# Kernel tuning notes

Hardware: AMD Instinct MI355X
Metric: run time of the kernel (lower is better)

Reference implementation:

```python
import jax, jax.numpy as jnp
import numpy as np

B, T, C, H, N = 2, 1024, 2048, 32, 64
LAYER_ID, N_LAYERS = 12, 24
EPS = 1e-5 * 8 ** 2  # GroupNorm eps = 1e-5 * head_size_divisor**2


def setup_inputs() -> dict:
    key = jax.random.key(0)
    ks = jax.random.split(key, 16)
    nrm = lambda i, shape, s: jax.random.normal(ks[i], shape, jnp.float32) * s
    r01 = LAYER_ID / (N_LAYERS - 1)
    r1a0 = 1.0 - LAYER_ID / N_LAYERS
    ddd = (jnp.arange(C, dtype=jnp.float32) / C)[None, None, :]
    nn_ = jnp.arange(C, dtype=jnp.float32) / (C - 1)
    decay_speed = -7.0 + 5.0 * nn_ ** (0.85 + r01 ** 0.5)
    lin_s = 1.0 / float(np.sqrt(C))
    inp = dict(
        x=nrm(0, (B, T, C), 1.0),
        v_first=nrm(1, (B, T, C), 1.0),
        shift_state=jnp.zeros((B, C), jnp.float32),
        wkv_state=jnp.zeros((B, H, N, N), jnp.float32),
        x_r=1.0 - ddd ** (0.2 * r1a0),
        x_w=1.0 - ddd ** (0.9 * r1a0),
        x_k=1.0 - (ddd ** (0.9 * r1a0) + 0.4 * r01),
        x_v=1.0 - (ddd ** (0.4 * r1a0) + 0.6 * r01),
        x_a=1.0 - ddd ** (0.9 * r1a0),
        x_g=1.0 - ddd ** (0.2 * r1a0),
        w0=decay_speed[None, None, :] + 0.5,
        w1=nrm(2, (C, 64), 0.05), w2=nrm(3, (64, C), 0.1),
        a0=jnp.zeros((1, 1, C), jnp.float32),
        a1=nrm(4, (C, 64), 0.05), a2=nrm(5, (64, C), 0.1),
        v0=jnp.ones((1, 1, C), jnp.float32),
        v1=nrm(6, (C, 32), 0.05), v2=nrm(7, (32, C), 0.1),
        g1=nrm(8, (C, 128), 0.05), g2=nrm(9, (128, C), 0.1),
        k_k=jnp.full((1, 1, C), 0.85, jnp.float32),
        k_a=jnp.ones((1, 1, C), jnp.float32),
        r_k=nrm(10, (H, N), 0.02),
        W_r=nrm(11, (C, C), lin_s), W_k=nrm(12, (C, C), lin_s),
        W_v=nrm(13, (C, C), lin_s), W_o=nrm(14, (C, C), lin_s),
        ln_w=jnp.ones((C,), jnp.float32), ln_b=jnp.zeros((C,), jnp.float32),
    )
    return inp


def _forward(x, v_first, shift_state, wkv_state, x_r, x_w, x_k, x_v, x_a, x_g,
             w0, w1, w2, a0, a1, a2, v0, v1, v2, g1, g2, k_k, k_a, r_k,
             W_r, W_k, W_v, W_o, ln_w, ln_b):
    # token shift
    xx = jnp.concatenate([shift_state[:, None, :], x[:, :-1]], axis=1) - x
    xr, xw, xk, xv, xa, xg = (x + xx * m for m in (x_r, x_w, x_k, x_v, x_a, x_g))
    r = xr @ W_r
    k = xk @ W_k
    v = xv @ W_v
    # log-decay (strictly negative)
    w_log = -jax.nn.softplus(-(w0 + jnp.tanh(xw @ w1) @ w2)) - 0.5
    # residual value mixing towards layer-0 v (layer_id > 0 branch)
    v = v + (v_first - v) * jax.nn.sigmoid(v0 + xv @ v1 @ v2)
    a = jax.nn.sigmoid(a0 + xa @ a1 @ a2)
    g = jax.nn.sigmoid(xg @ g1) @ g2
    # per-head L2-normalized removal key
    kk = (k * k_k).reshape(B, T, H, N)
    kk = kk / jnp.maximum(jnp.linalg.norm(kk, axis=-1, keepdims=True), 1e-12)
    k2 = k * (1.0 + (a - 1.0) * k_a)
    # time-major [T,B,H,N] for the scan
    tm = lambda t: t.reshape(B, T, H, N).transpose(1, 0, 2, 3)
    rs, ks_, vs = tm(r), tm(k2), tm(v)
    ws = jnp.exp(tm(w_log))               # per-channel decay in (0,1)
    a_in = -kk.transpose(1, 0, 2, 3)      # removal direction
    b_in = (kk * a.reshape(B, T, H, N)).transpose(1, 0, 2, 3)
    def step(S, t):  # S: [B,H,Nv,Nk]
        r_, k_, v_, w_, a_, b_ = t
        sa = jnp.einsum('bhvk,bhk->bhv', S, a_)
        S = S * w_[:, :, None, :] \
            + jnp.einsum('bhv,bhk->bhvk', sa, b_) \
            + jnp.einsum('bhv,bhk->bhvk', v_, k_)
        return S, jnp.einsum('bhvk,bhk->bhv', S, r_)
    S_final, o = jax.lax.scan(step, wkv_state, (rs, ks_, vs, ws, a_in, b_in))
    o = o.transpose(1, 0, 2, 3)           # [B,T,H,N]
    # GroupNorm with H groups over C channels (per-head normalization)
    mu = o.mean(-1, keepdims=True)
    var = ((o - mu) ** 2).mean(-1, keepdims=True)
    on = ((o - mu) / jnp.sqrt(var + EPS)).reshape(B, T, C) * ln_w + ln_b
    # rkv bonus term
    rr, kr, vr = r.reshape(B, T, H, N), k2.reshape(B, T, H, N), v.reshape(B, T, H, N)
    bonus = ((rr * kr * r_k).sum(-1, keepdims=True) * vr).reshape(B, T, C)
    out = ((on + bonus) * g) @ W_o
    return out


def reference(x, v_first, shift_state, wkv_state, x_r, x_w, x_k, x_v, x_a, x_g,
              w0, w1, w2, a0, a1, a2, v0, v1, v2, g1, g2, k_k, k_a, r_k,
              W_r, W_k, W_v, W_o, ln_w, ln_b):
    return _forward(x, v_first, shift_state, wkv_state, x_r, x_w, x_k, x_v, x_a, x_g,
                    w0, w1, w2, a0, a1, a2, v0, v1, v2, g1, g2, k_k, k_a, r_k,
                    W_r, W_k, W_v, W_o, ln_w, ln_b)
```

## Files before the change

### kernel.cpp

```cpp
#include <hip/hip_runtime.h>
#include <cstdint>
#include <cstddef>


#define DI __device__ __forceinline__
static constexpr int T_ = 1024, C_ = 2048, H_ = 32;

typedef __attribute__((ext_vector_type(8))) __bf16 bf16x8;
typedef __attribute__((ext_vector_type(4))) float f32x4;
typedef __attribute__((ext_vector_type(8))) unsigned short us8v;
typedef __attribute__((ext_vector_type(4))) unsigned short us4v;
typedef __attribute__((ext_vector_type(2))) unsigned short us2v;

DI float sig_(float z) { return 1.0f / (1.0f + expf(-z)); }

DI unsigned short f2bf(float f) {
  union { float f; uint32_t u; } v; v.f = f;
  uint32_t u = v.u;
  return (unsigned short)((u + 0x7FFFu + ((u >> 16) & 1u)) >> 16);
}
DI float bf2f(unsigned short h) {
  union { uint32_t u; float f; } v; v.u = ((uint32_t)h) << 16;
  return v.f;
}

DI float dpp_xor1_add(float x) {
  int r = __builtin_amdgcn_update_dpp(0, __float_as_int(x), 0xB1, 0xF, 0xF, true);
  return x + __int_as_float(r);
}
DI float dpp_xor2_add(float x) {
  int r = __builtin_amdgcn_update_dpp(0, __float_as_int(x), 0x4E, 0xF, 0xF, true);
  return x + __int_as_float(r);
}
DI float dpp_hm_add(float x) {
  int r = __builtin_amdgcn_update_dpp(0, __float_as_int(x), 0x141, 0xF, 0xF, true);
  return x + __int_as_float(r);
}
DI float dpp_mir_add(float x) {
  int r = __builtin_amdgcn_update_dpp(0, __float_as_int(x), 0x140, 0xF, 0xF, true);
  return x + __int_as_float(r);
}

DI void gload16(const float* g, float* l) {
  __builtin_amdgcn_global_load_lds(
      (const __attribute__((address_space(1))) uint32_t*)g,
      (__attribute__((address_space(3))) uint32_t*)l, 16, 0, 0);
}
DI void gload16u(const unsigned short* g, unsigned short* l) {
  __builtin_amdgcn_global_load_lds(
      (const __attribute__((address_space(1))) uint32_t*)g,
      (__attribute__((address_space(3))) uint32_t*)l, 16, 0, 0);
}
DI void gload4(const float* g, float* l) {
  __builtin_amdgcn_global_load_lds(
      (const __attribute__((address_space(1))) uint32_t*)g,
      (__attribute__((address_space(3))) uint32_t*)l, 4, 0, 0);
}

struct Job {
  const float* A; const float* W; float* C; const float* bias;
  const float* mixv; const float* x; const float* shift;
  int N, K, ntn, aact, epi, tile_end;
};
struct Jobs { Job j[7]; };

__global__ __launch_bounds__(256) void gemm_oracle(Jobs P) {
  __shared__ float As[64][33];
  __shared__ float Ws[32][65];
  int bx = blockIdx.x, ji = 0;
  while (bx >= P.j[ji].tile_end) ++ji;
  Job J = P.j[ji];
  int tix = bx - (ji ? P.j[ji - 1].tile_end : 0);
  int mt = tix / J.ntn, nt = tix % J.ntn;
  int m0 = mt * 64, n0 = nt * 64;
  int tid = threadIdx.x, tx = tid & 15, ty = tid >> 4;
  float acc[4][4] = {};
  for (int k0 = 0; k0 < J.K; k0 += 32) {
    #pragma unroll
    for (int p = 0; p < 8; ++p) {
      int idx = p * 256 + tid;
      int r = idx >> 5, kc = idx & 31;
      int m = m0 + r, k = k0 + kc;
      float a;
      if (J.mixv) {
        float xv = J.x[(size_t)m * C_ + k];
        int t = m & (T_ - 1);
        float xp = (t == 0) ? J.shift[(size_t)(m >> 10) * C_ + k]
                            : J.x[(size_t)(m - 1) * C_ + k];
        a = xv + (xp - xv) * J.mixv[k];
      } else {
        a = J.A[(size_t)m * J.K + k];
        if (J.aact == 1) a = tanhf(a);
        else if (J.aact == 2) a = sig_(a);
      }
      As[r][kc] = a;
    }
    #pragma unroll
    for (int p = 0; p < 8; ++p) {
      int idx = p * 256 + tid;
      int kr = idx >> 6, nc = idx & 63;
      int n = n0 + nc;
      Ws[kr][nc] = (n < J.N) ? J.W[(size_t)(k0 + kr) * J.N + n] : 0.0f;
    }
    __syncthreads();
    #pragma unroll 4
    for (int kc = 0; kc < 32; ++kc) {
      float av[4], bv[4];
      #pragma unroll
      for (int i = 0; i < 4; ++i) av[i] = As[ty * 4 + i][kc];
      #pragma unroll
      for (int jn = 0; jn < 4; ++jn) bv[jn] = Ws[kc][tx * 4 + jn];
      #pragma unroll
      for (int i = 0; i < 4; ++i)
        #pragma unroll
        for (int jn = 0; jn < 4; ++jn) acc[i][jn] += av[i] * bv[jn];
    }
    __syncthreads();
  }
  #pragma unroll
  for (int i = 0; i < 4; ++i) {
    int rw = m0 + ty * 4 + i;
    #pragma unroll
    for (int jn = 0; jn < 4; ++jn) {
      int col = n0 + tx * 4 + jn;
      if (col < J.N) {
        float v = acc[i][jn];
        if (J.epi == 1) v = sig_(J.bias[col] + v);
        else if (J.epi == 2) v = 0.60653065971263342f * sig_(J.bias[col] + v);
        if (J.epi == 3) ((unsigned short*)J.C)[(size_t)rw * J.N + col] = f2bf(v);
        else            J.C[(size_t)rw * J.N + col] = v;
      }
    }
  }
}

struct TJob { const float* src; unsigned short* dh; unsigned short* dl; int N, ntn, tile_end; };
struct TJobs { TJob j[8]; };

__global__ __launch_bounds__(256) void wtrans(TJobs P) {
  __shared__ float t[64][65];
  int bx = blockIdx.x, ji = 0;
  while (bx >= P.j[ji].tile_end) ++ji;
  TJob J = P.j[ji];
  int tix = bx - (ji ? P.j[ji - 1].tile_end : 0);
  int kt = tix / J.ntn, nt = tix % J.ntn;
  int k0 = kt * 64, n0 = nt * 64;
  int tid = threadIdx.x;
  #pragma unroll
  for (int p = 0; p < 16; ++p) {
    int flat = p * 256 + tid;
    int r = flat >> 6, c = flat & 63;
    int n = n0 + c;
    t[r][c] = (n < J.N) ? J.src[(size_t)(k0 + r) * J.N + n] : 0.0f;
  }
  __syncthreads();
  #pragma unroll
  for (int p = 0; p < 8; ++p) {
    int flat = p * 256 + tid;
    int rr = flat >> 5, cc = (flat & 31) * 2;
    if (n0 + rr < J.N) {
      float w0v = t[cc][rr], w1v = t[cc + 1][rr];
      unsigned short h0 = f2bf(w0v), h1 = f2bf(w1v);
      us2v oh, ol;
      oh.x = h0; oh.y = h1;
      ol.x = f2bf(w0v - bf2f(h0));
      ol.y = f2bf(w1v - bf2f(h1));
      size_t off = (size_t)(n0 + rr) * 2048 + k0 + cc;
      *(us2v*)(J.dh + off) = oh;
      *(us2v*)(J.dl + off) = ol;
    }
  }
}

struct GJob {
  const float* A; const unsigned short* Wh; const unsigned short* Wl; float* C;
  const float* mixv; const float* shift;
  int N, K, ntn, kbeg, kend, atomicC, tile_end;
};
struct GJobs { GJob j[8]; };

__global__ __launch_bounds__(256, 2) void gemm_w256(GJobs P) {
  __shared__ unsigned short Ash[128][40];
  __shared__ unsigned short Asl[128][40];
  __shared__ unsigned short Bsh[256][32];
  __shared__ unsigned short Bsl[256][32];
  int bx = blockIdx.x, ji = 0;
  while (bx >= P.j[ji].tile_end) ++ji;
  GJob J = P.j[ji];
  int tix = bx - (ji ? P.j[ji - 1].tile_end : 0);
  int mt = tix / J.ntn, nt = tix % J.ntn;
  int m0 = mt * 128, n0 = nt * 256;
  int tid = threadIdx.x;
  int lane = tid & 63, wid = tid >> 6;
  int wr = wid >> 1, wc = wid & 1;
  int l15 = lane & 15, lg = lane >> 4;
  f32x4 acc[4][8] = {};

  int sr = tid >> 3, skq = tid & 7;
  float ax[4][4], aq[4][4], amv[4];

  auto loadA = [&](int k0) {
    int kk = k0 + skq * 4;
    if (J.mixv) *(float4*)amv = *(const float4*)(J.mixv + kk);
    #pragma unroll
    for (int p = 0; p < 4; ++p) {
      int m = m0 + p * 32 + sr;
      const float* xp0 = J.A + (size_t)m * J.K + kk;
      *(float4*)ax[p] = *(const float4*)xp0;
      if (J.mixv) {
        const float* pp = ((m & (T_ - 1)) == 0)
            ? (J.shift + (size_t)(m >> 10) * C_ + kk)
            : (xp0 - C_);
        *(float4*)aq[p] = *(const float4*)pp;
      }
    }
  };
  auto writeA = [&]() {
    #pragma unroll
    for (int p = 0; p < 4; ++p) {
      us4v oh, ol;
      #pragma unroll
      for (int q = 0; q < 4; ++q) {
        float va = J.mixv ? (ax[p][q] + (aq[p][q] - ax[p][q]) * amv[q]) : ax[p][q];
        unsigned short hq = f2bf(va);
        oh[q] = hq;
        ol[q] = f2bf(va - bf2f(hq));
      }
      int r = p * 32 + sr;
      *(us4v*)&Ash[r][skq * 4] = oh;
      *(us4v*)&Asl[r][skq * 4] = ol;
    }
  };
  auto stageB = [&](int k0) {
    #pragma unroll
    for (int j = 0; j < 4; ++j) {
      int r0 = wid * 64 + j * 16;
      int rdst = r0 + (lane >> 2);
      int nrow = n0 + rdst;
      if (nrow >= J.N) nrow = J.N - 1;
      int ssrc = (lane & 3) ^ ((rdst >> 1) & 3);
      size_t gofs = (size_t)nrow * J.K + k0 + ssrc * 8;
      gload16u(J.Wh + gofs, &Bsh[r0][0]);
      gload16u(J.Wl + gofs, &Bsl[r0][0]);
    }
  };

  loadA(J.kbeg);
  stageB(J.kbeg);
  writeA();
  asm volatile("s_waitcnt vmcnt(0)" ::: "memory");
  __syncthreads();

  for (int k0 = J.kbeg; k0 < J.kend; k0 += 32) {
    bool more = (k0 + 32 < J.kend);
    if (more) loadA(k0 + 32);
    bf16x8 afh[4], afl[4];
    #pragma unroll
    for (int i = 0; i < 4; ++i) {
      int rr = wr * 64 + i * 16 + l15;
      afh[i] = __builtin_bit_cast(bf16x8, *(const us8v*)&Ash[rr][lg * 8]);
      afl[i] = __builtin_bit_cast(bf16x8, *(const us8v*)&Asl[rr][lg * 8]);
    }
    #pragma unroll
    for (int jn = 0; jn < 8; ++jn) {
      int rb = wc * 128 + jn * 16 + l15;
      int sl = (lg ^ ((rb >> 1) & 3)) * 8;
      bf16x8 bh = __builtin_bit_cast(bf16x8, *(const us8v*)&Bsh[rb][sl]);
      bf16x8 bl = __builtin_bit_cast(bf16x8, *(const us8v*)&Bsl[rb][sl]);
      #pragma unroll
      for (int i = 0; i < 4; ++i) {
        acc[i][jn] = __builtin_amdgcn_mfma_f32_16x16x32_bf16(afh[i], bh, acc[i][jn], 0, 0, 0);
        acc[i][jn] = __builtin_amdgcn_mfma_f32_16x16x32_bf16(afl[i], bh, acc[i][jn], 0, 0, 0);
        acc[i][jn] = __builtin_amdgcn_mfma_f32_16x16x32_bf16(afh[i], bl, acc[i][jn], 0, 0, 0);
      }
    }
    __syncthreads();
    if (more) { stageB(k0 + 32); writeA(); }
    asm volatile("s_waitcnt vmcnt(0)" ::: "memory");
    __syncthreads();
  }

  int orow0 = m0 + wr * 64 + 4 * lg;
  int ocol0 = n0 + wc * 128 + l15;
  #pragma unroll
  for (int i = 0; i < 4; ++i) {
    #pragma unroll
    for (int jn = 0; jn < 8; ++jn) {
      int col = ocol0 + jn * 16;
      if (col < J.N) {
        #pragma unroll
        for (int rr = 0; rr < 4; ++rr) {
          size_t idx = (size_t)(orow0 + i * 16 + rr) * J.N + col;
          float v = acc[i][jn][rr];
          if (J.atomicC) atomicAdd(&J.C[idx], v);
          else           J.C[idx] = v;
        }
      }
    }
  }
}

__global__ __launch_bounds__(64) void prescan(
    float* __restrict__ kio, float* __restrict__ vio,
    float* __restrict__ amat_ain, float* __restrict__ vmix_bin,
    const float* __restrict__ vfirst,
    const float* __restrict__ k_k, const float* __restrict__ k_a) {
  __shared__ float red[64];
  int bid = blockIdx.x, tid = threadIdx.x;
  int h = bid & (H_ - 1);
  size_t base = (size_t)bid * 64 + tid;
  int cc = h * 64 + tid;
  float kv = kio[base];
  float kkv = kv * k_k[cc];
  red[tid] = kkv * kkv;
  __syncthreads();
  for (int s = 32; s > 0; s >>= 1) { if (tid < s) red[tid] += red[tid + s]; __syncthreads(); }
  float nrm = fmaxf(sqrtf(red[0]), 1e-12f);
  float kkn = kkv / nrm;
  float av = amat_ain[base];
  float vmv = vmix_bin[base];
  float vv = vio[base];
  kio[base] = kv * (1.0f + (av - 1.0f) * k_a[cc]);
  vio[base] = vv + (vfirst[base] - vv) * vmv;
  amat_ain[base] = -kkn;
  vmix_bin[base] = kkn * av;
}

static constexpr int CH = 8;

#define LOADSTEP(BUF, S_, Aa, Ww, Kk, Bb, Rr, Vt)                  \
  {                                                                \
    *(float4*)&Aa[0] = *(const float4*)&lds[BUF][3][S_][kb];       \
    *(float4*)&Ww[0] = *(const float4*)&lds[BUF][2][S_][kb];       \
    *(float4*)&Kk[0] = *(const float4*)&lds[BUF][1][S_][kb];       \
    *(float4*)&Bb[0] = *(const float4*)&lds[BUF][4][S_][kb];       \
    *(float4*)&Rr[0] = *(const float4*)&lds[BUF][0][S_][kb];       \
    Vt = vtl[BUF][S_][vl];                                         \
  }

#define COMPSTEP(Aa, Ww, Kk, Bb, Rr, Vt, TIDX)                              \
  {                                                                         \
    float p0 = S[0] * Aa[0], p1 = S[1] * Aa[1];                             \
    p0 = fmaf(S[2], Aa[2], p0);                                             \
    p1 = fmaf(S[3], Aa[3], p1);                                             \
    float sa = p0 + p1;                                                     \
    sa = dpp_xor1_add(sa);                                                  \
    sa = dpp_xor2_add(sa);                                                  \
    sa = dpp_hm_add(sa);                                                    \
    sa = dpp_mir_add(sa);                                                   \
    S[0] = fmaf(S[0], Ww[0], fmaf(Vt, Kk[0], sa * Bb[0]));                  \
    S[1] = fmaf(S[1], Ww[1], fmaf(Vt, Kk[1], sa * Bb[1]));                  \
    S[2] = fmaf(S[2], Ww[2], fmaf(Vt, Kk[2], sa * Bb[2]));                  \
    S[3] = fmaf(S[3], Ww[3], fmaf(Vt, Kk[3], sa * Bb[3]));                  \
    float y0 = S[0] * Rr[0], y1 = S[1] * Rr[1];                             \
    y0 = fmaf(S[2], Rr[2], y0);                                             \
    y1 = fmaf(S[3], Rr[3], y1);                                             \
    float y = y0 + y1;                                                      \
    y = dpp_xor1_add(y);                                                    \
    y = dpp_xor2_add(y);                                                    \
    y = dpp_hm_add(y);                                                      \
    y = dpp_mir_add(y);                                                     \
    if (kq == 0) obf[bh + (size_t)(TIDX)*2048 + v0 + vl] = f2bf(y);         \
  }

__global__ __launch_bounds__(64) void wkv_scan_v6(
    const float* __restrict__ r, const float* __restrict__ k2,
    const float* __restrict__ w, const float* __restrict__ ain,
    const float* __restrict__ bin, const float* __restrict__ vp,
    const float* __restrict__ sInit, unsigned short* __restrict__ obf) {
  __shared__ float lds[2][5][CH][64];
  __shared__ float vtl[2][16][4];
  int D = blockIdx.x;
  int chain = (D & 7) + 8 * (D >> 7);
  int vblk = (D >> 3) & 15;
  int b = chain >> 5, h = chain & 31;
  int v0 = vblk * 4;
  int lane = threadIdx.x;
  int vl = lane >> 4, kq = lane & 15;
  int kb = kq * 4;
  size_t bh = (size_t)(b * T_) * 2048 + (size_t)h * 64;

  float S[4];
  {
    const float* sp = sInit + (((size_t)chain * 64 + v0 + vl) * 64) + kb;
    float4 s0 = *(const float4*)sp;
    S[0] = s0.x; S[1] = s0.y; S[2] = s0.z; S[3] = s0.w;
  }

  const float* arr[5] = {r, k2, w, ain, bin};

  auto stage = [&](int buf, int t0) {
    #pragma unroll
    for (int a = 0; a < 5; ++a) {
      #pragma unroll
      for (int jj = 0; jj < 2; ++jj) {
        size_t gofs = bh + (size_t)(t0 + jj * 4 + (lane >> 4)) * 2048 + (lane & 15) * 4;
        gload16(arr[a] + gofs, &lds[buf][a][jj * 4][0]);
      }
    }
    {
      int tt = t0 + (lane >> 2);
      if (tt > T_ - 1) tt = T_ - 1;
      size_t gofs = bh + (size_t)tt * 2048 + v0 + (lane & 3);
      gload4(vp + gofs, &vtl[buf][0][0]);
    }
  };

  stage(0, 0);
  asm volatile("s_waitcnt vmcnt(0)" ::: "memory");

  float A0[4], W0[4], K0[4], B0[4], R0[4], vt0;
  float A1[4], W1[4], K1[4], B1[4], R1[4], vt1;

  for (int c = 0; c < T_ / CH; ++c) {
    int cur = c & 1;
    if (c + 1 < T_ / CH) stage(cur ^ 1, (c + 1) * CH);
    int t0 = c * CH;
    LOADSTEP(cur, 0, A0, W0, K0, B0, R0, vt0);
    #pragma unroll 2
    for (int s = 0; s < CH; s += 2) {
      LOADSTEP(cur, s + 1, A1, W1, K1, B1, R1, vt1);
      COMPSTEP(A0, W0, K0, B0, R0, vt0, t0 + s);
      if (s + 2 < CH) LOADSTEP(cur, s + 2, A0, W0, K0, B0, R0, vt0);
      COMPSTEP(A1, W1, K1, B1, R1, vt1, t0 + s + 1);
    }
    asm volatile("s_waitcnt vmcnt(0)" ::: "memory");
  }
}

__global__ __launch_bounds__(64) void post(
    const unsigned short* __restrict__ obf, const float* __restrict__ r,
    const float* __restrict__ k2, const float* __restrict__ vp,
    const unsigned short* __restrict__ gbf, const float* __restrict__ r_k,
    const float* __restrict__ lnw, const float* __restrict__ lnb,
    float* __restrict__ afin) {
  __shared__ float red[64];
  int bid = blockIdx.x, tid = threadIdx.x;
  int h = bid & 31;
  size_t base = (size_t)bid * 64 + tid;
  int cc = h * 64 + tid;
  float ov = bf2f(obf[base]);
  red[tid] = ov; __syncthreads();
  for (int s = 32; s > 0; s >>= 1) { if (tid < s) red[tid] += red[tid + s]; __syncthreads(); }
  float mu = red[0] * (1.0f / 64.0f);
  __syncthreads();
  float dv = ov - mu;
  red[tid] = dv * dv; __syncthreads();
  for (int s = 32; s > 0; s >>= 1) { if (tid < s) red[tid] += red[tid + s]; __syncthreads(); }
  float var = red[0] * (1.0f / 64.0f);
  __syncthreads();
  float on = dv * rsqrtf(var + 6.4e-4f) * lnw[cc] + lnb[cc];
  float pr = r[base] * k2[base] * r_k[cc];
  red[tid] = pr; __syncthreads();
  for (int s = 32; s > 0; s >>= 1) { if (tid < s) red[tid] += red[tid + s]; __syncthreads(); }
  float dot = red[0];
  float val = (on + dot * vp[base]) * bf2f(gbf[base]);
  afin[base] = val;
}

static constexpr size_t KB = 1024;
static constexpr size_t O_R    = 0;
static constexpr size_t O_K    = 16384;
static constexpr size_t O_V    = 32768;
static constexpr size_t O_WDEC = 49152;
static constexpr size_t O_AMAT = 65536;
static constexpr size_t O_VMIX = 81920;
static constexpr size_t O_AIN  = O_AMAT;
static constexpr size_t O_BIN  = O_VMIX;
static constexpr size_t O_AFIN = O_VMIX;
static constexpr size_t O_WRT_H = 49152, O_WRT_L = 57344;
static constexpr size_t O_WKT_H = 65536, O_WKT_L = 73728;
static constexpr size_t O_WVT_H = 81920, O_WVT_L = 90112;
static constexpr size_t O_W1T_H = 98304, O_W1T_L = 98560;
static constexpr size_t O_A1T_H = 98816, O_A1T_L = 99072;
static constexpr size_t O_V1T_H = 99328, O_V1T_L = 99456;
static constexpr size_t O_G1T_H = 99584, O_G1T_L = 100096;
static constexpr size_t O_WOT_H = 0, O_WOT_L = 8192;

extern "C" void kernel_launch(void* const* d_in, const int* in_sizes, int n_in,
                              void* d_out, int out_size, void* d_ws, size_t ws_size,
                              hipStream_t stream) {
  const float* x      = (const float*)d_in[0];
  const float* vfirst = (const float*)d_in[1];
  const float* shift  = (const float*)d_in[2];
  const float* wkv0   = (const float*)d_in[3];
  const float* x_r = (const float*)d_in[4];
  const float* x_w = (const float*)d_in[5];
  const float* x_k = (const float*)d_in[6];
  const float* x_v = (const float*)d_in[7];
  const float* x_a = (const float*)d_in[8];
  const float* x_g = (const float*)d_in[9];
  const float* w0 = (const float*)d_in[10];
  const float* w1 = (const float*)d_in[11];
  const float* w2 = (const float*)d_in[12];
  const float* a0 = (const float*)d_in[13];
  const float* a1 = (const float*)d_in[14];
  const float* a2 = (const float*)d_in[15];
  const float* v0 = (const float*)d_in[16];
  const float* v1 = (const float*)d_in[17];
  const float* v2 = (const float*)d_in[18];
  const float* g1 = (const float*)d_in[19];
  const float* g2 = (const float*)d_in[20];
  const float* k_k = (const float*)d_in[21];
  const float* k_a = (const float*)d_in[22];
  const float* r_k = (const float*)d_in[23];
  const float* W_r = (const float*)d_in[24];
  const float* W_k = (const float*)d_in[25];
  const float* W_v = (const float*)d_in[26];
  const float* W_o = (const float*)d_in[27];
  const float* ln_w = (const float*)d_in[28];
  const float* ln_b = (const float*)d_in[29];

  char* ws = (char*)d_ws;
  auto F = [&](size_t kb) { return (float*)(ws + kb * KB); };
  auto U = [&](size_t kb) { return (unsigned short*)(ws + kb * KB); };
  float* outp = (float*)d_out;
  unsigned short* gbf = (unsigned short*)d_out;
  unsigned short* obf = (unsigned short*)((char*)d_out + 8192 * KB);
  float* HW2 = (float*)((char*)d_out + 8192 * KB);
  float* HA2 = (float*)((char*)d_out + 8704 * KB);
  float* HV2 = (float*)((char*)d_out + 9216 * KB);
  float* HG2 = (float*)((char*)d_out + 9472 * KB);

  {
    TJobs TG{};
    int cum = 0, i = 0;
    auto addT = [&](const float* src, size_t hkb, size_t lkb, int N) {
      int ntn = (N + 63) / 64;
      cum += 32 * ntn;
      TG.j[i++] = TJob{src, U(hkb), U(lkb), N, ntn, cum};
    };
    addT(W_r, O_WRT_H, O_WRT_L, 2048);
    addT(W_k, O_WKT_H, O_WKT_L, 2048);
    addT(W_v, O_WVT_H, O_WVT_L, 2048);
    addT(w1, O_W1T_H, O_W1T_L, 64);
    addT(a1, O_A1T_H, O_A1T_L, 64);
    addT(v1, O_V1T_H, O_V1T_L, 32);
    addT(g1, O_G1T_H, O_G1T_L, 128);
    wtrans<<<dim3(cum), dim3(256), 0, stream>>>(TG);
  }

  {
    GJobs G{};
    int cum = 0, i = 0;
    auto add = [&](size_t hkb, size_t lkb, float* Cp, const float* mixv, int N) {
      int ntn = (N + 255) / 256;
      cum += 16 * ntn;
      G.j[i++] = GJob{x, U(hkb), U(lkb), Cp, mixv, shift, N, 2048, ntn, 0, 2048, 0, cum};
    };
    add(O_WRT_H, O_WRT_L, F(O_R), x_r, 2048);
    add(O_WKT_H, O_WKT_L, F(O_K), x_k, 2048);
    add(O_WVT_H, O_WVT_L, F(O_V), x_v, 2048);
    add(O_W1T_H, O_W1T_L, HW2, x_w, 64);
    add(O_A1T_H, O_A1T_L, HA2, x_a, 64);
    add(O_V1T_H, O_V1T_L, HV2, x_v, 32);
    add(O_G1T_H, O_G1T_L, HG2, x_g, 128);
    gemm_w256<<<dim3(cum), dim3(256), 0, stream>>>(G);
  }

  {
    Jobs G{};
    int cum = 0, i = 0;
    auto add = [&](const float* A, const float* W, float* C, const float* bias,
                   int K, int aact, int epi) {
      cum += 32 * 32;
      G.j[i++] = Job{A, W, C, bias, nullptr, nullptr, nullptr, 2048, K, 32, aact, epi, cum};
    };
    add(HW2, w2, F(O_WDEC), w0, 64, 1, 2);
    add(HA2, a2, F(O_AMAT), a0, 64, 0, 1);
    add(HV2, v2, F(O_VMIX), v0, 32, 0, 1);
    add(HG2, g2, (float*)gbf, nullptr, 128, 2, 3);
    gemm_oracle<<<dim3(cum), dim3(256), 0, stream>>>(G);
  }

  prescan<<<dim3(65536), dim3(64), 0, stream>>>(F(O_K), F(O_V), F(O_AMAT), F(O_VMIX),
                                                vfirst, k_k, k_a);

  wkv_scan_v6<<<dim3(1024), dim3(64), 0, stream>>>(F(O_R), F(O_K), F(O_WDEC), F(O_AIN),
                                                   F(O_BIN), F(O_V), wkv0, obf);

  post<<<dim3(65536), dim3(64), 0, stream>>>(obf, F(O_R), F(O_K), F(O_V),
                                             gbf, r_k, ln_w, ln_b, F(O_AFIN));

  hipMemsetAsync(d_out, 0, (size_t)16384 * KB, stream);

  {
    TJobs TO{};
    TO.j[0] = TJob{W_o, U(O_WOT_H), U(O_WOT_L), 2048, 32, 1024};
    wtrans<<<dim3(1024), dim3(256), 0, stream>>>(TO);
  }

  {
    GJobs G{};
    G.j[0] = GJob{F(O_AFIN), U(O_WOT_H), U(O_WOT_L), outp, nullptr, nullptr,
                  2048, 2048, 8, 0, 1024, 1, 128};
    G.j[1] = GJob{F(O_AFIN), U(O_WOT_H), U(O_WOT_L), outp, nullptr, nullptr,
                  2048, 2048, 8, 1024, 2048, 1, 256};
    gemm_w256<<<dim3(256), dim3(256), 0, stream>>>(G);
  }

  (void)in_sizes; (void)n_in; (void)out_size; (void)ws_size;
}
```

Measured before the change: 830.3 us.

## Split WKV scan state across more lanes and use wave shuffles in pre/post kernels

The WKV scan kernel now gives each lane 2 state elements instead of 4. A 64-wide k dimension is reduced across two half-waves with DPP plus permlane32_swap, and each 256-thread block covers 8 v-rows with cooperative staging and a block barrier per chunk. This shortens the per-step serial FMA chain and spreads the recurrence over more waves, at the cost of an extra cross-lane op and __syncthreads per chunk. The prescan and post kernels pack 4 heads per 256-thread block and swap LDS tree reductions for xor-shuffle reductions. Post also computes variance as E[x^2]-mu^2 in a single pass, which can lose a little precision.

Result: slower. 858.8 us (+3.4%).

```diff
diff --git a/kernel.cpp b/kernel.cpp
--- a/kernel.cpp
+++ b/kernel.cpp
@@ -11,6 +11,7 @@
 typedef __attribute__((ext_vector_type(8))) unsigned short us8v;
 typedef __attribute__((ext_vector_type(4))) unsigned short us4v;
 typedef __attribute__((ext_vector_type(2))) unsigned short us2v;
+typedef __attribute__((ext_vector_type(2))) int i32x2;
 
 DI float sig_(float z) { return 1.0f / (1.0f + expf(-z)); }
 
@@ -39,6 +40,11 @@
 DI float dpp_mir_add(float x) {
   int r = __builtin_amdgcn_update_dpp(0, __float_as_int(x), 0x140, 0xF, 0xF, true);
   return x + __int_as_float(r);
+}
+DI float cross32_add(float x) {
+  i32x2 p = __builtin_amdgcn_permlane32_swap(__float_as_int(x), __float_as_int(x),
+                                             false, false);
+  return __int_as_float(p.x) + __int_as_float(p.y);
 }
 
 DI void gload16(const float* g, float* l) {
@@ -300,22 +306,22 @@
   }
 }
 
-__global__ __launch_bounds__(64) void prescan(
+__global__ __launch_bounds__(256) void prescan(
     float* __restrict__ kio, float* __restrict__ vio,
     float* __restrict__ amat_ain, float* __restrict__ vmix_bin,
     const float* __restrict__ vfirst,
     const float* __restrict__ k_k, const float* __restrict__ k_a) {
-  __shared__ float red[64];
-  int bid = blockIdx.x, tid = threadIdx.x;
-  int h = bid & (H_ - 1);
-  size_t base = (size_t)bid * 64 + tid;
-  int cc = h * 64 + tid;
+  int gh = blockIdx.x * 4 + (threadIdx.x >> 6);
+  int lane = threadIdx.x & 63;
+  int h = gh & (H_ - 1);
+  size_t base = (size_t)gh * 64 + lane;
+  int cc = h * 64 + lane;
   float kv = kio[base];
   float kkv = kv * k_k[cc];
-  red[tid] = kkv * kkv;
-  __syncthreads();
-  for (int s = 32; s > 0; s >>= 1) { if (tid < s) red[tid] += red[tid + s]; __syncthreads(); }
-  float nrm = fmaxf(sqrtf(red[0]), 1e-12f);
+  float ss = kkv * kkv;
+  ss += __shfl_xor(ss, 1);  ss += __shfl_xor(ss, 2);  ss += __shfl_xor(ss, 4);
+  ss += __shfl_xor(ss, 8);  ss += __shfl_xor(ss, 16); ss += __shfl_xor(ss, 32);
+  float nrm = fmaxf(sqrtf(ss), 1e-12f);
   float kkn = kkv / nrm;
   float av = amat_ain[base];
   float vmv = vmix_bin[base];
@@ -328,89 +334,78 @@
 
 static constexpr int CH = 8;
 
-#define LOADSTEP(BUF, S_, Aa, Ww, Kk, Bb, Rr, Vt)                  \
-  {                                                                \
-    *(float4*)&Aa[0] = *(const float4*)&lds[BUF][3][S_][kb];       \
-    *(float4*)&Ww[0] = *(const float4*)&lds[BUF][2][S_][kb];       \
-    *(float4*)&Kk[0] = *(const float4*)&lds[BUF][1][S_][kb];       \
-    *(float4*)&Bb[0] = *(const float4*)&lds[BUF][4][S_][kb];       \
-    *(float4*)&Rr[0] = *(const float4*)&lds[BUF][0][S_][kb];       \
-    Vt = vtl[BUF][S_][vl];                                         \
-  }
-
-#define COMPSTEP(Aa, Ww, Kk, Bb, Rr, Vt, TIDX)                              \
-  {                                                                         \
-    float p0 = S[0] * Aa[0], p1 = S[1] * Aa[1];                             \
-    p0 = fmaf(S[2], Aa[2], p0);                                             \
-    p1 = fmaf(S[3], Aa[3], p1);                                             \
-    float sa = p0 + p1;                                                     \
-    sa = dpp_xor1_add(sa);                                                  \
-    sa = dpp_xor2_add(sa);                                                  \
-    sa = dpp_hm_add(sa);                                                    \
-    sa = dpp_mir_add(sa);                                                   \
-    S[0] = fmaf(S[0], Ww[0], fmaf(Vt, Kk[0], sa * Bb[0]));                  \
-    S[1] = fmaf(S[1], Ww[1], fmaf(Vt, Kk[1], sa * Bb[1]));                  \
-    S[2] = fmaf(S[2], Ww[2], fmaf(Vt, Kk[2], sa * Bb[2]));                  \
-    S[3] = fmaf(S[3], Ww[3], fmaf(Vt, Kk[3], sa * Bb[3]));                  \
-    float y0 = S[0] * Rr[0], y1 = S[1] * Rr[1];                             \
-    y0 = fmaf(S[2], Rr[2], y0);                                             \
-    y1 = fmaf(S[3], Rr[3], y1);                                             \
-    float y = y0 + y1;                                                      \
-    y = dpp_xor1_add(y);                                                    \
-    y = dpp_xor2_add(y);                                                    \
-    y = dpp_hm_add(y);                                                      \
-    y = dpp_mir_add(y);                                                     \
-    if (kq == 0) obf[bh + (size_t)(TIDX)*2048 + v0 + vl] = f2bf(y);         \
-  }
-
-__global__ __launch_bounds__(64) void wkv_scan_v6(
+#define LOADSTEP(BUF, S_, Aa, Ww, Kk, Bb, Rr, Vt)                    \
+  {                                                                  \
+    *(float2*)&Aa[0] = *(const float2*)&lds[BUF][3][S_][kb];         \
+    *(float2*)&Ww[0] = *(const float2*)&lds[BUF][2][S_][kb];         \
+    *(float2*)&Kk[0] = *(const float2*)&lds[BUF][1][S_][kb];         \
+    *(float2*)&Bb[0] = *(const float2*)&lds[BUF][4][S_][kb];         \
+    *(float2*)&Rr[0] = *(const float2*)&lds[BUF][0][S_][kb];         \
+    Vt = vtl[BUF][S_][vr];                                           \
+  }
+
+#define COMPSTEP(Aa, Ww, Kk, Bb, Rr, Vt, TIDX)                       \
+  {                                                                  \
+    float pa = fmaf(S1, Aa[1], S0 * Aa[0]);                          \
+    pa = dpp_xor1_add(pa); pa = dpp_xor2_add(pa);                    \
+    pa = dpp_hm_add(pa);   pa = dpp_mir_add(pa);                     \
+    float sa = cross32_add(pa);                                      \
+    S0 = fmaf(S0, Ww[0], fmaf(Vt, Kk[0], sa * Bb[0]));               \
+    S1 = fmaf(S1, Ww[1], fmaf(Vt, Kk[1], sa * Bb[1]));               \
+    float py = fmaf(S1, Rr[1], S0 * Rr[0]);                          \
+    py = dpp_xor1_add(py); py = dpp_xor2_add(py);                    \
+    py = dpp_hm_add(py);   py = dpp_mir_add(py);                     \
+    float y = cross32_add(py);                                       \
+    if (kq == 0) obf[bh + (size_t)(TIDX)*2048 + v0 + vr] = f2bf(y);  \
+  }
+
+__global__ __launch_bounds__(256) void wkv_scan_v7(
     const float* __restrict__ r, const float* __restrict__ k2,
     const float* __restrict__ w, const float* __restrict__ ain,
     const float* __restrict__ bin, const float* __restrict__ vp,
     const float* __restrict__ sInit, unsigned short* __restrict__ obf) {
   __shared__ float lds[2][5][CH][64];
-  __shared__ float vtl[2][16][4];
+  __shared__ float vtl[2][CH][8];
   int D = blockIdx.x;
-  int chain = (D & 7) + 8 * (D >> 7);
-  int vblk = (D >> 3) & 15;
+  int chain = (D & 7) + 8 * (D >> 6);
+  int vblk = (D >> 3) & 7;
   int b = chain >> 5, h = chain & 31;
-  int v0 = vblk * 4;
-  int lane = threadIdx.x;
-  int vl = lane >> 4, kq = lane & 15;
-  int kb = kq * 4;
+  int v0 = vblk * 8;
+  int tid = threadIdx.x;
+  int wid = tid >> 6, lane = tid & 63;
+  int vl = (lane >> 4) & 1;
+  int kq = (lane & 15) | ((lane >> 5) << 4);
+  int kb = kq * 2;
+  int vr = 2 * wid + vl;
   size_t bh = (size_t)(b * T_) * 2048 + (size_t)h * 64;
 
-  float S[4];
+  float S0, S1;
   {
-    const float* sp = sInit + (((size_t)chain * 64 + v0 + vl) * 64) + kb;
-    float4 s0 = *(const float4*)sp;
-    S[0] = s0.x; S[1] = s0.y; S[2] = s0.z; S[3] = s0.w;
+    const float* sp = sInit + (((size_t)chain * 64 + v0 + vr) * 64) + kb;
+    float2 s = *(const float2*)sp;
+    S0 = s.x; S1 = s.y;
   }
 
   const float* arr[5] = {r, k2, w, ain, bin};
 
   auto stage = [&](int buf, int t0) {
-    #pragma unroll
-    for (int a = 0; a < 5; ++a) {
-      #pragma unroll
-      for (int jj = 0; jj < 2; ++jj) {
-        size_t gofs = bh + (size_t)(t0 + jj * 4 + (lane >> 4)) * 2048 + (lane & 15) * 4;
-        gload16(arr[a] + gofs, &lds[buf][a][jj * 4][0]);
-      }
-    }
-    {
-      int tt = t0 + (lane >> 2);
-      if (tt > T_ - 1) tt = T_ - 1;
-      size_t gofs = bh + (size_t)tt * 2048 + v0 + (lane & 3);
+    for (int d = wid; d < 10; d += 4) {
+      int a = d >> 1, hf = d & 1;
+      size_t gofs = bh + (size_t)(t0 + hf * 4 + (lane >> 4)) * 2048 + (lane & 15) * 4;
+      gload16(arr[a] + gofs, &lds[buf][a][hf * 4][0]);
+    }
+    if (wid == 2) {
+      size_t gofs = bh + (size_t)(t0 + (lane >> 3)) * 2048 + v0 + (lane & 7);
       gload4(vp + gofs, &vtl[buf][0][0]);
     }
   };
 
   stage(0, 0);
   asm volatile("s_waitcnt vmcnt(0)" ::: "memory");
-
-  float A0[4], W0[4], K0[4], B0[4], R0[4], vt0;
-  float A1[4], W1[4], K1[4], B1[4], R1[4], vt1;
+  __syncthreads();
+
+  float A0[2], W0[2], K0[2], B0[2], R0[2], vt0;
+  float A1[2], W1[2], K1[2], B1[2], R1[2], vt1;
 
   for (int c = 0; c < T_ / CH; ++c) {
     int cur = c & 1;
@@ -425,36 +420,34 @@
       COMPSTEP(A1, W1, K1, B1, R1, vt1, t0 + s + 1);
     }
     asm volatile("s_waitcnt vmcnt(0)" ::: "memory");
-  }
-}
-
-__global__ __launch_bounds__(64) void post(
+    __syncthreads();
+  }
+}
+
+__global__ __launch_bounds__(256) void post(
     const unsigned short* __restrict__ obf, const float* __restrict__ r,
     const float* __restrict__ k2, const float* __restrict__ vp,
     const unsigned short* __restrict__ gbf, const float* __restrict__ r_k,
     const float* __restrict__ lnw, const float* __restrict__ lnb,
     float* __restrict__ afin) {
-  __shared__ float red[64];
-  int bid = blockIdx.x, tid = threadIdx.x;
-  int h = bid & 31;
-  size_t base = (size_t)bid * 64 + tid;
-  int cc = h * 64 + tid;
+  int gh = blockIdx.x * 4 + (threadIdx.x >> 6);
+  int lane = threadIdx.x & 63;
+  int h = gh & 31;
+  size_t base = (size_t)gh * 64 + lane;
+  int cc = h * 64 + lane;
   float ov = bf2f(obf[base]);
-  red[tid] = ov; __syncthreads();
-  for (int s = 32; s > 0; s >>= 1) { if (tid < s) red[tid] += red[tid + s]; __syncthreads(); }
-  float mu = red[0] * (1.0f / 64.0f);
-  __syncthreads();
-  float dv = ov - mu;
-  red[tid] = dv * dv; __syncthreads();
-  for (int s = 32; s > 0; s >>= 1) { if (tid < s) red[tid] += red[tid + s]; __syncthreads(); }
-  float var = red[0] * (1.0f / 64.0f);
-  __syncthreads();
-  float on = dv * rsqrtf(var + 6.4e-4f) * lnw[cc] + lnb[cc];
   float pr = r[base] * k2[base] * r_k[cc];
-  red[tid] = pr; __syncthreads();
-  for (int s = 32; s > 0; s >>= 1) { if (tid < s) red[tid] += red[tid + s]; __syncthreads(); }
-  float dot = red[0];
-  float val = (on + dot * vp[base]) * bf2f(gbf[base]);
+  float so = ov, so2 = ov * ov, sd = pr;
+  #pragma unroll
+  for (int d = 1; d <= 32; d <<= 1) {
+    so  += __shfl_xor(so, d);
+    so2 += __shfl_xor(so2, d);
+    sd  += __shfl_xor(sd, d);
+  }
+  float mu = so * (1.0f / 64.0f);
+  float var = so2 * (1.0f / 64.0f) - mu * mu;
+  float on = (ov - mu) * rsqrtf(var + 6.4e-4f) * lnw[cc] + lnb[cc];
+  float val = (on + sd * vp[base]) * bf2f(gbf[base]);
   afin[base] = val;
 }
 
@@ -573,14 +566,14 @@
     gemm_oracle<<<dim3(cum), dim3(256), 0, stream>>>(G);
   }
 
-  prescan<<<dim3(65536), dim3(64), 0, stream>>>(F(O_K), F(O_V), F(O_AMAT), F(O_VMIX),
-                                                vfirst, k_k, k_a);
-
-  wkv_scan_v6<<<dim3(1024), dim3(64), 0, stream>>>(F(O_R), F(O_K), F(O_WDEC), F(O_AIN),
+  prescan<<<dim3(16384), dim3(256), 0, stream>>>(F(O_K), F(O_V), F(O_AMAT), F(O_VMIX),
+                                                 vfirst, k_k, k_a);
+
+  wkv_scan_v7<<<dim3(512), dim3(256), 0, stream>>>(F(O_R), F(O_K), F(O_WDEC), F(O_AIN),
                                                    F(O_BIN), F(O_V), wkv0, obf);
 
-  post<<<dim3(65536), dim3(64), 0, stream>>>(obf, F(O_R), F(O_K), F(O_V),
-                                             gbf, r_k, ln_w, ln_b, F(O_AFIN));
+  post<<<dim3(16384), dim3(256), 0, stream>>>(obf, F(O_R), F(O_K), F(O_V),
+                                              gbf, r_k, ln_w, ln_b, F(O_AFIN));
 
   hipMemsetAsync(d_out, 0, (size_t)16384 * KB, stream);
 
```
